# Kernel optimization log

Hardware: AMD Instinct MI355X
Metric: run time of the kernel (lower is better)

Reference implementation:

```python
import jax, jax.numpy as jnp
import numpy as np

E, H = 1024, 16


def setup_inputs() -> dict:
    key = jax.random.key(0)
    k1, k2, k3, k4 = jax.random.split(key, 4)
    B, L = 4, 2048
    embeddings = jax.random.normal(k1, (B, L, E), dtype=jnp.float32)
    mask = jax.random.randint(k2, (B, L, L), 0, 2) == 1  # True = masked out
    # Params (torch Linear y = x @ W.T; we store already-transposed [in, out])
    W_qkv = jax.random.normal(k3, (E, 3 * E), dtype=jnp.float32) * 0.02
    W_out = jax.random.normal(k4, (E, E), dtype=jnp.float32) * 0.02
    return {"embeddings": embeddings, "mask": mask, "W_qkv": W_qkv, "W_out": W_out}


def reference(embeddings, mask, W_qkv, W_out):
    B, L, E_ = embeddings.shape
    A = E_ // H
    scale = A ** (-0.5)
    qkv = embeddings @ W_qkv                       # [B, L, 3E]
    qkv = qkv.reshape(B, L, H, 3 * A).transpose(0, 2, 1, 3)  # [B, H, L, 3A]
    q, k, v = jnp.split(qkv, 3, axis=-1)           # each [B, H, L, A]
    scores = jnp.einsum('bhqa,bhka->bhqk', q, k) * scale  # [B, H, L, L]
    m = mask[:, None, :, :]                        # [B, 1, L, L]
    fully = jnp.all(m, axis=-1, keepdims=True)     # rows with every key masked
    scores = jnp.where(m, -jnp.inf, scores)
    scores = jnp.where(fully, 0.0, scores)         # keep softmax finite
    attn = jax.nn.softmax(scores, axis=-1)
    attn = jnp.where(fully, 0.0, attn)             # == torch nan_to_num(0)
    values = jnp.einsum('bhqk,bhka->bhqa', attn, v)  # [B, H, L, A]
    values = values.transpose(0, 2, 1, 3).reshape(B, L, E_)
    return values @ W_out
```

## Files before the change

kernel.cpp:

```cpp
#include <hip/hip_runtime.h>
#include <hip/hip_bf16.h>

#define B_   4
#define L_   2048
#define E_   1024
#define H_   16
#define T_   8192
#define K_   1024

typedef __attribute__((ext_vector_type(8))) short bf16x8;
typedef __attribute__((ext_vector_type(4))) float f32x4;
typedef __attribute__((ext_vector_type(4))) unsigned u32x4;

#define CSC_ (0.125f * 1.44269504f)

__device__ __forceinline__ ushort f2b(float f) {
    union { float f; unsigned u; } x; x.f = f;
    unsigned r = (x.u + 0x7fffu + ((x.u >> 16) & 1u)) >> 16;
    return (ushort)r;
}

__device__ __forceinline__ float fexp2(float x) {
#if __has_builtin(__builtin_amdgcn_exp2f)
    return __builtin_amdgcn_exp2f(x);
#else
    return __expf(x * 0.69314718056f);
#endif
}

__device__ __forceinline__ unsigned pack2bf(float a, float b) {
#if __has_builtin(__builtin_amdgcn_cvt_pk_bf16_f32)
    auto t = __builtin_amdgcn_cvt_pk_bf16_f32(a, b);
    return __builtin_bit_cast(unsigned, t);
#else
    unsigned ua = __builtin_bit_cast(unsigned, a) + 0x8000u;
    unsigned ub = __builtin_bit_cast(unsigned, b) + 0x8000u;
    return __builtin_amdgcn_perm(ub, ua, 0x07060302);
#endif
}

#define GLD_LDS16(gp, lp) __builtin_amdgcn_global_load_lds( \
    (const __attribute__((address_space(1))) void*)(gp), \
    (__attribute__((address_space(3))) void*)(lp), 16, 0, 0)

__global__ void detect_mask_layout(const unsigned char* __restrict__ m, int* flag) {
    __shared__ int s;
    if (threadIdx.x == 0) s = 0;
    __syncthreads();
    int found = 0;
    for (int i = threadIdx.x; i < 4096; i += 256)
        if ((i & 3) != 0 && m[i] != 0) found = 1;
    if (found) atomicOr(&s, 1);
    __syncthreads();
    if (threadIdx.x == 0) *flag = s;
}

__global__ void pack_mask(const void* __restrict__ mraw, const int* __restrict__ flag,
                          unsigned* __restrict__ tbits) {
    int row  = blockIdx.x;
    int lane = threadIdx.x & 63;
    int wave = threadIdx.x >> 6;
    int isByte = *flag;
    int b = row >> 11, q = row & 2047;
    const unsigned char* mb = (const unsigned char*)mraw;
    const int*           mi = (const int*)mraw;
    long long base = (long long)row * L_;
    for (int w = wave; w < 32; w += 4) {
        int idx = w * 64 + lane;
        int v = isByte ? (int)mb[base + idx] : mi[base + idx];
        unsigned long long word = __ballot(v == 0);
        if (lane == 0) {
            tbits[((size_t)b * 64 + 2 * w)     * 2048 + q] = (unsigned)word;
            tbits[((size_t)b * 64 + 2 * w + 1) * 2048 + q] = (unsigned)(word >> 32);
        }
    }
}

__global__ __launch_bounds__(256) void conv_bf16(const float* __restrict__ in,
                                                 ushort* __restrict__ out) {
    int i = blockIdx.x * 256 + threadIdx.x;
    float4 v = ((const float4*)in)[i];
    uint2 o;
    o.x = (unsigned)f2b(v.x) | ((unsigned)f2b(v.y) << 16);
    o.y = (unsigned)f2b(v.z) | ((unsigned)f2b(v.w) << 16);
    ((uint2*)out)[i] = o;
}

__global__ __launch_bounds__(256) void transpose_conv(const float* __restrict__ in,
        ushort* __restrict__ out, int R, int Cn) {
    __shared__ float t[32][33];
    int c0 = blockIdx.x * 32, r0 = blockIdx.y * 32;
    int x = threadIdx.x & 31, y = threadIdx.x >> 5;
#pragma unroll
    for (int k = 0; k < 4; ++k)
        t[y + k * 8][x] = in[(size_t)(r0 + y + k * 8) * Cn + c0 + x];
    __syncthreads();
#pragma unroll
    for (int k = 0; k < 4; ++k)
        out[(size_t)(c0 + y + k * 8) * R + r0 + x] = f2b(t[x][y + k * 8]);
}

template<int NDIM, int MODE>
__global__ __launch_bounds__(256) void gemm_bf16(
        const ushort* __restrict__ Ab, const ushort* __restrict__ Bt,
        float* __restrict__ Cg, ushort* __restrict__ Qb,
        ushort* __restrict__ Kb, ushort* __restrict__ Vt) {
    __shared__ ushort As[128 * 64];
    __shared__ ushort Bs[128 * 64];
    const int tid = threadIdx.x;
    const int wv = tid >> 6, ln = tid & 63;
    const int bn = blockIdx.x * 128, bm = blockIdx.y * 128;
    const int wm = (wv & 1) * 64, wn = (wv >> 1) * 64;
    const int row16 = ln & 15, quad = ln >> 4;
    const int cg8 = (((ln & 7) ^ (ln >> 3)) * 8);

    f32x4 acc[4][4];
#pragma unroll
    for (int i = 0; i < 4; ++i)
#pragma unroll
        for (int j = 0; j < 4; ++j) acc[i][j] = (f32x4){0.f, 0.f, 0.f, 0.f};

    for (int k0 = 0; k0 < K_; k0 += 64) {
        __syncthreads();
#pragma unroll
        for (int it = 0; it < 4; ++it) {
            int rA = wv * 32 + it * 8 + (ln >> 3);
            GLD_LDS16(Ab + (size_t)(bm + rA) * K_ + k0 + cg8, &As[(wv * 32 + it * 8) * 64]);
            GLD_LDS16(Bt + (size_t)(bn + rA) * K_ + k0 + cg8, &Bs[(wv * 32 + it * 8) * 64]);
        }
        __syncthreads();
#pragma unroll
        for (int ks = 0; ks < 2; ++ks) {
            const int ch = (((ks * 4 + quad) ^ (ln & 7)) * 8);
            bf16x8 af[4], bf[4];
#pragma unroll
            for (int i = 0; i < 4; ++i)
                af[i] = *(const bf16x8*)&As[(wm + i * 16 + row16) * 64 + ch];
#pragma unroll
            for (int j = 0; j < 4; ++j)
                bf[j] = *(const bf16x8*)&Bs[(wn + j * 16 + row16) * 64 + ch];
#pragma unroll
            for (int i = 0; i < 4; ++i)
#pragma unroll
                for (int j = 0; j < 4; ++j)
                    acc[i][j] = __builtin_amdgcn_mfma_f32_16x16x32_bf16(
                        af[i], bf[j], acc[i][j], 0, 0, 0);
        }
    }

    if (MODE == 0) {
#pragma unroll
        for (int i = 0; i < 4; ++i)
#pragma unroll
            for (int j = 0; j < 4; ++j) {
                int col = bn + wn + j * 16 + row16;
#pragma unroll
                for (int r = 0; r < 4; ++r) {
                    int row = bm + wm + i * 16 + quad * 4 + r;
                    Cg[(size_t)row * NDIM + col] = acc[i][j][r];
                }
            }
    } else {
#pragma unroll
        for (int j = 0; j < 4; ++j) {
            int col = bn + wn + j * 16 + row16;
            int h = col / 192, w = col - h * 192;
            int sel = w >> 6, a = w & 63;
            float qs = (sel == 0) ? CSC_ : 1.0f;
#pragma unroll
            for (int i = 0; i < 4; ++i)
#pragma unroll
                for (int r = 0; r < 4; ++r) {
                    int rowg = bm + wm + i * 16 + quad * 4 + r;
                    int b = rowg >> 11, l = rowg & 2047;
                    ushort v = f2b(acc[i][j][r] * qs);
                    size_t bh = (size_t)(b * H_ + h);
                    if (sel == 0)      Qb[(bh * L_ + l) * 64 + a] = v;
                    else if (sel == 1) Kb[(bh * L_ + l) * 64 + a] = v;
                    else {
                        int k5 = l & 31;
                        int lp = (l & ~31) | (2 * (k5 & 15) + (k5 >> 4));
                        Vt[(bh * 64 + a) * L_ + lp] = v;
                    }
                }
        }
    }
}

__global__ __launch_bounds__(512, 4) void attn_mfma(
        const ushort* __restrict__ Qb, const ushort* __restrict__ Kb,
        const ushort* __restrict__ Vt, const unsigned* __restrict__ tbits,
        ushort* __restrict__ vals) {
    __shared__ ushort KV[6][4096];

    const int tid = threadIdx.x, wv = tid >> 6, ln = tid & 63;
    const int bh = blockIdx.x, b = bh >> 4, h = bh & 15;
    const int q0 = blockIdx.y * 256;
    const int row16 = ln & 15, quad = ln >> 4;
    const int lh = ln >> 3, ll = ln & 7;
    const int cg8 = ((ll ^ lh) * 8);

    const ushort* Kg = Kb + (size_t)bh * L_ * 64;
    const ushort* Vg = Vt + (size_t)bh * 64 * L_;

    const int wk = wv & 3;
    const bool isK = (wv < 4);
    const int vc4 = ll ^ lh;
    const ushort* vstage = Vg + (size_t)(wk * 8 + lh + 32 * (vc4 >> 2)) * L_ + (vc4 & 3) * 8;
    const ushort* kstage = Kg + (size_t)(wk * 8 + lh) * 64 + cg8;

    ushort* lds = &KV[0][0];

    {
        const ushort* Qgw = Qb + ((size_t)bh * L_ + q0 + wv * 32) * 64;
#pragma unroll
        for (int it = 0; it < 4; ++it)
            GLD_LDS16(Qgw + (size_t)(it * 8 + lh) * 64 + cg8,
                      lds + (wv * 32 + it * 8) * 64);
    }
    __syncthreads();
    bf16x8 aq[2][2];
#pragma unroll
    for (int rg = 0; rg < 2; ++rg)
#pragma unroll
        for (int ks = 0; ks < 2; ++ks)
            aq[rg][ks] = *(const bf16x8*)&lds[(wv * 32 + rg * 16 + row16) * 64 +
                                              (((ks * 4 + quad) ^ (row16 & 7)) * 8)];
    __syncthreads();

    if (isK) {
        GLD_LDS16(kstage,               &KV[0][(wk * 8) * 64]);
        GLD_LDS16(kstage + 2048,        &KV[0][(32 + wk * 8) * 64]);
        GLD_LDS16(kstage + 4096,        &KV[1][(wk * 8) * 64]);
        GLD_LDS16(kstage + 4096 + 2048, &KV[1][(32 + wk * 8) * 64]);
        kstage += 8192;
    } else {
        GLD_LDS16(vstage,      &KV[3][(wk * 8) * 64]);
        GLD_LDS16(vstage + 32, &KV[3][(32 + wk * 8) * 64]);
        GLD_LDS16(vstage + 64, &KV[4][(wk * 8) * 64]);
        GLD_LDS16(vstage + 96, &KV[4][(32 + wk * 8) * 64]);
        vstage += 128;
    }

    bf16x8 vone;
#pragma unroll
    for (int i = 0; i < 8; ++i) vone[i] = (short)0x3F80;
    const f32x4 zf = (f32x4){0.f, 0.f, 0.f, 0.f};

    f32x4 oacc[2][4], lacc[2];
#pragma unroll
    for (int rg = 0; rg < 2; ++rg) {
        lacc[rg] = zf;
#pragma unroll
        for (int t = 0; t < 4; ++t) oacc[rg][t] = zf;
    }

    const unsigned* mptr = tbits + (size_t)b * 64 * 2048 + (q0 + wv * 32 + row16);

    auto qk = [&](const ushort* kbuf, int sub, f32x4 (&s)[2][2]) {
        __builtin_amdgcn_s_setprio(1);
#pragma unroll
        for (int ks = 0; ks < 2; ++ks) {
            bf16x8 bk[2];
#pragma unroll
            for (int t = 0; t < 2; ++t)
                bk[t] = *(const bf16x8*)&kbuf[(sub * 32 + t * 16 + row16) * 64 +
                                              (((ks * 4 + quad) ^ (row16 & 7)) * 8)];
#pragma unroll
            for (int rg = 0; rg < 2; ++rg)
#pragma unroll
                for (int t = 0; t < 2; ++t)
                    s[rg][t] = __builtin_amdgcn_mfma_f32_16x16x32_bf16(
                        bk[t], aq[rg][ks], ks ? s[rg][t] : zf, 0, 0, 0);
        }
        __builtin_amdgcn_s_setprio(0);
    };

    auto sm_pv = [&](f32x4 (&sa)[2][2], unsigned mlo, unsigned mhi,
                     const ushort* vbuf, int sub) {
        bf16x8 ap[2];
#pragma unroll
        for (int rg = 0; rg < 2; ++rg) {
            unsigned wr = rg ? mhi : mlo;
            u32x4 pw;
#pragma unroll
            for (int r = 0; r < 4; ++r) {
                unsigned sh = wr >> (quad * 4 + r);
                unsigned pk = pack2bf(fexp2(sa[rg][0][r]), fexp2(sa[rg][1][r]));
                pk &= (sh & 0x00010001u) * 0xFFFFu;
                pw[r] = pk;
            }
            ap[rg] = __builtin_bit_cast(bf16x8, pw);
        }
        bf16x8 bv[4];
#pragma unroll
        for (int t = 0; t < 4; ++t)
            bv[t] = *(const bf16x8*)&vbuf[(sub * 32 + (t & 1) * 16 + row16) * 64 +
                                          ((((t >> 1) * 4 + quad) ^ (row16 & 7)) * 8)];
        __builtin_amdgcn_s_setprio(1);
#pragma unroll
        for (int rg = 0; rg < 2; ++rg) {
            lacc[rg] = __builtin_amdgcn_mfma_f32_16x16x32_bf16(
                ap[rg], vone, lacc[rg], 0, 0, 0);
#pragma unroll
            for (int t = 0; t < 4; ++t)
                oacc[rg][t] = __builtin_amdgcn_mfma_f32_16x16x32_bf16(
                    ap[rg], bv[t], oacc[rg][t], 0, 0, 0);
        }
        __builtin_amdgcn_s_setprio(0);
    };

    auto iter = [&](const ushort* kb, const ushort* vb,
                    ushort* kn, ushort* vn, bool st) {
        unsigned m0lo = mptr[0],    m0hi = mptr[16];
        unsigned m1lo = mptr[2048], m1hi = mptr[2048 + 16];
        mptr += 4096;
        __builtin_amdgcn_sched_barrier(0);
        if (st) {
            if (isK) {
                GLD_LDS16(kstage,        kn + (wk * 8) * 64);
                GLD_LDS16(kstage + 2048, kn + (32 + wk * 8) * 64);
                kstage += 4096;
            } else {
                GLD_LDS16(vstage,      vn + (wk * 8) * 64);
                GLD_LDS16(vstage + 32, vn + (32 + wk * 8) * 64);
                vstage += 64;
            }
        }
        f32x4 s0[2][2];
        qk(kb, 0, s0);
        sm_pv(s0, m0lo, m0hi, vb, 0);
        f32x4 s1[2][2];
        qk(kb, 1, s1);
        sm_pv(s1, m1lo, m1hi, vb, 1);
        asm volatile("s_waitcnt vmcnt(2)" ::: "memory");
        __builtin_amdgcn_s_barrier();
        __builtin_amdgcn_sched_barrier(0);
    };

    asm volatile("s_waitcnt vmcnt(2)" ::: "memory");
    __builtin_amdgcn_s_barrier();
    __builtin_amdgcn_sched_barrier(0);

    for (int g = 0; g < 10; ++g) {
        iter(KV[0], KV[3], KV[2], KV[5], true);
        iter(KV[1], KV[4], KV[0], KV[3], true);
        iter(KV[2], KV[5], KV[1], KV[4], true);
    }
    iter(KV[0], KV[3], KV[2], KV[5], false);
    iter(KV[1], KV[4], KV[0], KV[3], false);

#pragma unroll
    for (int rg = 0; rg < 2; ++rg)
#pragma unroll
        for (int r = 0; r < 4; ++r) {
            float l = lacc[rg][r];
            float inv = (l > 0.f) ? 1.0f / l : 0.f;
            int qrow = q0 + wv * 32 + rg * 16 + quad * 4 + r;
            size_t base = ((size_t)b * L_ + qrow) * E_ + h * 64;
#pragma unroll
            for (int t = 0; t < 4; ++t)
                vals[base + t * 16 + row16] = f2b(oacc[rg][t][r] * inv);
        }
}

extern "C" void kernel_launch(void* const* d_in, const int* in_sizes, int n_in,
                              void* d_out, int out_size, void* d_ws, size_t ws_size,
                              hipStream_t stream) {
    const float* emb  = (const float*)d_in[0];
    const void*  mask = d_in[1];
    const float* wqkv = (const float*)d_in[2];
    const float* wout = (const float*)d_in[3];
    float* out = (float*)d_out;

    char* ws = (char*)d_ws;
    const size_t NEED = 4096ull + 2097152ull + 2ull * 46137344ull;
    if (ws_size < NEED) return;

    int* flag = (int*)ws;
    unsigned* tbits = (unsigned*)(ws + 4096);
    ushort* embb  = (ushort*)(ws + 4096 + 2097152);
    ushort* Wqkvt = embb  + 8388608;
    ushort* Wott  = Wqkvt + 3145728;
    ushort* Qb    = Wott  + 1048576;
    ushort* Kb    = Qb    + 8388608;
    ushort* Vt    = Kb    + 8388608;
    ushort* vals  = Vt    + 8388608;

    detect_mask_layout<<<1, 256, 0, stream>>>((const unsigned char*)mask, flag);
    pack_mask<<<T_, 256, 0, stream>>>(mask, flag, tbits);
    conv_bf16<<<8192, 256, 0, stream>>>(emb, embb);
    transpose_conv<<<dim3(96, 32), 256, 0, stream>>>(wqkv, Wqkvt, 1024, 3072);
    transpose_conv<<<dim3(32, 32), 256, 0, stream>>>(wout, Wott, 1024, 1024);
    gemm_bf16<3072, 1><<<dim3(24, 64), 256, 0, stream>>>(
        embb, Wqkvt, nullptr, Qb, Kb, Vt);
    attn_mfma<<<dim3(64, 8), 512, 0, stream>>>(Qb, Kb, Vt, tbits, vals);
    gemm_bf16<1024, 0><<<dim3(8, 64), 256, 0, stream>>>(
        vals, Wott, out, nullptr, nullptr, nullptr);
}
```

Measured before the change: 357.1 us.

## Double-buffer GEMM LDS tiles with 32-wide K steps to overlap loads

Rewrites the bf16 GEMM main loop to use two LDS buffers, each holding a 32-wide K slice, in place of one 64-wide buffer. The next slice is issued to global-to-LDS while MFMAs run on the current one, with one barrier per step. It also sets launch bounds to 4 blocks per CU and changes the LDS swizzle to match the narrower rows. This trades twice as many K iterations and barriers for overlap of memory latency with compute.

```diff
diff --git a/kernel.cpp b/kernel.cpp
--- a/kernel.cpp
+++ b/kernel.cpp
@@ -101,18 +101,31 @@
 }
 
 template<int NDIM, int MODE>
-__global__ __launch_bounds__(256) void gemm_bf16(
+__global__ __launch_bounds__(256, 4) void gemm_bf16(
         const ushort* __restrict__ Ab, const ushort* __restrict__ Bt,
         float* __restrict__ Cg, ushort* __restrict__ Qb,
         ushort* __restrict__ Kb, ushort* __restrict__ Vt) {
-    __shared__ ushort As[128 * 64];
-    __shared__ ushort Bs[128 * 64];
+    __shared__ ushort As[2][128 * 32];
+    __shared__ ushort Bs[2][128 * 32];
     const int tid = threadIdx.x;
     const int wv = tid >> 6, ln = tid & 63;
     const int bn = blockIdx.x * 128, bm = blockIdx.y * 128;
     const int wm = (wv & 1) * 64, wn = (wv >> 1) * 64;
     const int row16 = ln & 15, quad = ln >> 4;
-    const int cg8 = (((ln & 7) ^ (ln >> 3)) * 8);
+
+    const int rr = ln >> 2;
+    const int cc8 = (((ln & 3) ^ (rr & 3)) * 8);
+
+    const ushort* Ag = Ab + (size_t)(bm + wv * 32 + rr) * K_ + cc8;
+    const ushort* Bg = Bt + (size_t)(bn + wv * 32 + rr) * K_ + cc8;
+
+    auto stage = [&](int k0, int buf) {
+#pragma unroll
+        for (int g = 0; g < 2; ++g) {
+            GLD_LDS16(Ag + (size_t)(g * 16) * K_ + k0, &As[buf][(wv * 32 + g * 16) * 32]);
+            GLD_LDS16(Bg + (size_t)(g * 16) * K_ + k0, &Bs[buf][(wv * 32 + g * 16) * 32]);
+        }
+    };
 
     f32x4 acc[4][4];
 #pragma unroll
@@ -120,32 +133,34 @@
 #pragma unroll
         for (int j = 0; j < 4; ++j) acc[i][j] = (f32x4){0.f, 0.f, 0.f, 0.f};
 
-    for (int k0 = 0; k0 < K_; k0 += 64) {
+    const int ch = (quad ^ (row16 & 3)) * 8;
+
+    auto compute = [&](const ushort* Ac, const ushort* Bc) {
+        bf16x8 af[4], bf[4];
+#pragma unroll
+        for (int i = 0; i < 4; ++i)
+            af[i] = *(const bf16x8*)&Ac[(wm + i * 16 + row16) * 32 + ch];
+#pragma unroll
+        for (int j = 0; j < 4; ++j)
+            bf[j] = *(const bf16x8*)&Bc[(wn + j * 16 + row16) * 32 + ch];
+#pragma unroll
+        for (int i = 0; i < 4; ++i)
+#pragma unroll
+            for (int j = 0; j < 4; ++j)
+                acc[i][j] = __builtin_amdgcn_mfma_f32_16x16x32_bf16(
+                    af[i], bf[j], acc[i][j], 0, 0, 0);
+    };
+
+    stage(0, 0);
+    __syncthreads();
+
+    for (int t = 0; t < 32; t += 2) {
+        stage((t + 1) * 32, 1);
+        compute(As[0], Bs[0]);
         __syncthreads();
-#pragma unroll
-        for (int it = 0; it < 4; ++it) {
-            int rA = wv * 32 + it * 8 + (ln >> 3);
-            GLD_LDS16(Ab + (size_t)(bm + rA) * K_ + k0 + cg8, &As[(wv * 32 + it * 8) * 64]);
-            GLD_LDS16(Bt + (size_t)(bn + rA) * K_ + k0 + cg8, &Bs[(wv * 32 + it * 8) * 64]);
-        }
+        if (t + 2 < 32) stage((t + 2) * 32, 0);
+        compute(As[1], Bs[1]);
         __syncthreads();
-#pragma unroll
-        for (int ks = 0; ks < 2; ++ks) {
-            const int ch = (((ks * 4 + quad) ^ (ln & 7)) * 8);
-            bf16x8 af[4], bf[4];
-#pragma unroll
-            for (int i = 0; i < 4; ++i)
-                af[i] = *(const bf16x8*)&As[(wm + i * 16 + row16) * 64 + ch];
-#pragma unroll
-            for (int j = 0; j < 4; ++j)
-                bf[j] = *(const bf16x8*)&Bs[(wn + j * 16 + row16) * 64 + ch];
-#pragma unroll
-            for (int i = 0; i < 4; ++i)
-#pragma unroll
-                for (int j = 0; j < 4; ++j)
-                    acc[i][j] = __builtin_amdgcn_mfma_f32_16x16x32_bf16(
-                        af[i], bf[j], acc[i][j], 0, 0, 0);
-        }
     }
 
     if (MODE == 0) {
```

Measured after the change: 353.3 us. Within noise of the previous version (-1.1%).

## Pipeline GEMM with triple-buffered A, double-buffered B, larger 256x128 tiles

Applied to the files above, without the earlier changes.

Rewrites the bf16 GEMM main loop to use 512-thread blocks with 256x128 output tiles. A tiles are triple-buffered and B tiles double-buffered in LDS, with global-to-LDS loads issued in phases interleaved with the MFMA work and gated by explicit vmcnt/lgkmcnt waits and barriers. It also raises wave priority around the MFMA blocks. The goal is to hide global load latency behind compute and to cut per-block sync overhead. The cost is more LDS (about 128KB per block), which limits occupancy, and more barriers per k-step.

```diff
diff --git a/kernel.cpp b/kernel.cpp
--- a/kernel.cpp
+++ b/kernel.cpp
@@ -100,59 +100,114 @@
         out[(size_t)(c0 + y + k * 8) * R + r0 + x] = f2b(t[x][y + k * 8]);
 }
 
+#define ASZ_ 16384
+#define BSZ_ 8192
+
 template<int NDIM, int MODE>
-__global__ __launch_bounds__(256) void gemm_bf16(
+__global__ __launch_bounds__(512, 2) void gemm_bf16(
         const ushort* __restrict__ Ab, const ushort* __restrict__ Bt,
         float* __restrict__ Cg, ushort* __restrict__ Qb,
         ushort* __restrict__ Kb, ushort* __restrict__ Vt) {
-    __shared__ ushort As[128 * 64];
-    __shared__ ushort Bs[128 * 64];
+    __shared__ ushort LDSm[3 * ASZ_ + 2 * BSZ_];
+    ushort* Asb = LDSm;
+    ushort* Bsb = LDSm + 3 * ASZ_;
+
     const int tid = threadIdx.x;
     const int wv = tid >> 6, ln = tid & 63;
-    const int bn = blockIdx.x * 128, bm = blockIdx.y * 128;
-    const int wm = (wv & 1) * 64, wn = (wv >> 1) * 64;
+    const int bn = blockIdx.x * 128, bm = blockIdx.y * 256;
+    const int wm = (wv & 1) * 128, wn = (wv >> 1) * 32;
     const int row16 = ln & 15, quad = ln >> 4;
-    const int cg8 = (((ln & 7) ^ (ln >> 3)) * 8);
-
-    f32x4 acc[4][4];
-#pragma unroll
-    for (int i = 0; i < 4; ++i)
-#pragma unroll
-        for (int j = 0; j < 4; ++j) acc[i][j] = (f32x4){0.f, 0.f, 0.f, 0.f};
-
-    for (int k0 = 0; k0 < K_; k0 += 64) {
-        __syncthreads();
-#pragma unroll
-        for (int it = 0; it < 4; ++it) {
-            int rA = wv * 32 + it * 8 + (ln >> 3);
-            GLD_LDS16(Ab + (size_t)(bm + rA) * K_ + k0 + cg8, &As[(wv * 32 + it * 8) * 64]);
-            GLD_LDS16(Bt + (size_t)(bn + rA) * K_ + k0 + cg8, &Bs[(wv * 32 + it * 8) * 64]);
-        }
-        __syncthreads();
-#pragma unroll
-        for (int ks = 0; ks < 2; ++ks) {
-            const int ch = (((ks * 4 + quad) ^ (ln & 7)) * 8);
-            bf16x8 af[4], bf[4];
-#pragma unroll
-            for (int i = 0; i < 4; ++i)
-                af[i] = *(const bf16x8*)&As[(wm + i * 16 + row16) * 64 + ch];
-#pragma unroll
-            for (int j = 0; j < 4; ++j)
-                bf[j] = *(const bf16x8*)&Bs[(wn + j * 16 + row16) * 64 + ch];
-#pragma unroll
-            for (int i = 0; i < 4; ++i)
-#pragma unroll
-                for (int j = 0; j < 4; ++j)
-                    acc[i][j] = __builtin_amdgcn_mfma_f32_16x16x32_bf16(
-                        af[i], bf[j], acc[i][j], 0, 0, 0);
+
+    const int lh = ln >> 3, ll = ln & 7;
+    const int sw8 = (ll ^ lh) * 8;
+    const ushort* Ag = Ab + (size_t)(bm + wv * 8 + lh) * K_ + sw8;
+    const ushort* Bg = Bt + (size_t)(bn + wv * 8 + lh) * K_ + sw8;
+
+    auto stA2 = [&](int k0, ushort* dst, int rb) {
+#pragma unroll
+        for (int r = 0; r < 2; ++r)
+            GLD_LDS16(Ag + (size_t)((rb + r) * 64) * K_ + k0,
+                      dst + ((rb + r) * 64 + wv * 8) * 64);
+    };
+    auto stB2 = [&](int k0, ushort* dst) {
+#pragma unroll
+        for (int r = 0; r < 2; ++r)
+            GLD_LDS16(Bg + (size_t)(r * 64) * K_ + k0,
+                      dst + (r * 64 + wv * 8) * 64);
+    };
+
+    f32x4 acc[8][2];
+#pragma unroll
+    for (int i = 0; i < 8; ++i)
+#pragma unroll
+        for (int j = 0; j < 2; ++j) acc[i][j] = (f32x4){0.f, 0.f, 0.f, 0.f};
+
+    stA2(0, Asb, 0); stA2(0, Asb, 2);
+    stB2(0, Bsb);
+    stA2(64, Asb + ASZ_, 0); stA2(64, Asb + ASZ_, 2);
+    asm volatile("s_waitcnt vmcnt(4)" ::: "memory");
+    __builtin_amdgcn_s_barrier();
+    __builtin_amdgcn_sched_barrier(0);
+
+    for (int t = 0; t < 16; ++t) {
+        const ushort* Ar = Asb + (t % 3) * ASZ_;
+        const ushort* Br = Bsb + (t & 1) * BSZ_;
+        ushort* Ast = Asb + ((t + 2) % 3) * ASZ_;
+        ushort* Bst = Bsb + ((t + 1) & 1) * BSZ_;
+        const int kA = (t + 2) * 64, kB = (t + 1) * 64;
+        bf16x8 bfr[2][2];
+#pragma unroll
+        for (int p = 0; p < 4; ++p) {
+            bf16x8 af[2][2];
+#pragma unroll
+            for (int di = 0; di < 2; ++di)
+#pragma unroll
+                for (int ks = 0; ks < 2; ++ks) {
+                    int row = wm + (2 * p + di) * 16 + row16;
+                    af[di][ks] = *(const bf16x8*)&Ar[row * 64 +
+                                     (((ks * 4 + quad) ^ (row16 & 7)) * 8)];
+                }
+            if (p == 0) {
+#pragma unroll
+                for (int j = 0; j < 2; ++j)
+#pragma unroll
+                    for (int ks = 0; ks < 2; ++ks) {
+                        int row = wn + j * 16 + row16;
+                        bfr[j][ks] = *(const bf16x8*)&Br[row * 64 +
+                                         (((ks * 4 + quad) ^ (row16 & 7)) * 8)];
+                    }
+            }
+            if (p == 0 && t < 15) stB2(kB, Bst);
+            if (p == 1 && t < 14) stA2(kA, Ast, 0);
+            if (p == 2 && t < 14) stA2(kA, Ast, 2);
+            __builtin_amdgcn_sched_barrier(0);
+            __builtin_amdgcn_s_barrier();
+            asm volatile("s_waitcnt lgkmcnt(0)" ::: "memory");
+            __builtin_amdgcn_sched_barrier(0);
+            __builtin_amdgcn_s_setprio(1);
+#pragma unroll
+            for (int ks = 0; ks < 2; ++ks)
+#pragma unroll
+                for (int di = 0; di < 2; ++di)
+#pragma unroll
+                    for (int j = 0; j < 2; ++j)
+                        acc[2 * p + di][j] = __builtin_amdgcn_mfma_f32_16x16x32_bf16(
+                            af[di][ks], bfr[j][ks], acc[2 * p + di][j], 0, 0, 0);
+            __builtin_amdgcn_s_setprio(0);
+            if (p == 3) {
+                if (t < 14)       { asm volatile("s_waitcnt vmcnt(4)" ::: "memory"); }
+                else if (t == 14) { asm volatile("s_waitcnt vmcnt(0)" ::: "memory"); }
+            }
+            __builtin_amdgcn_s_barrier();
+            __builtin_amdgcn_sched_barrier(0);
         }
     }
 
     if (MODE == 0) {
 #pragma unroll
-        for (int i = 0; i < 4; ++i)
-#pragma unroll
-            for (int j = 0; j < 4; ++j) {
+        for (int i = 0; i < 8; ++i)
+#pragma unroll
+            for (int j = 0; j < 2; ++j) {
                 int col = bn + wn + j * 16 + row16;
 #pragma unroll
                 for (int r = 0; r < 4; ++r) {
@@ -162,13 +217,13 @@
             }
     } else {
 #pragma unroll
-        for (int j = 0; j < 4; ++j) {
+        for (int j = 0; j < 2; ++j) {
             int col = bn + wn + j * 16 + row16;
             int h = col / 192, w = col - h * 192;
             int sel = w >> 6, a = w & 63;
             float qs = (sel == 0) ? CSC_ : 1.0f;
 #pragma unroll
-            for (int i = 0; i < 4; ++i)
+            for (int i = 0; i < 8; ++i)
 #pragma unroll
                 for (int r = 0; r < 4; ++r) {
                     int rowg = bm + wm + i * 16 + quad * 4 + r;
@@ -392,9 +447,9 @@
     conv_bf16<<<8192, 256, 0, stream>>>(emb, embb);
     transpose_conv<<<dim3(96, 32), 256, 0, stream>>>(wqkv, Wqkvt, 1024, 3072);
     transpose_conv<<<dim3(32, 32), 256, 0, stream>>>(wout, Wott, 1024, 1024);
-    gemm_bf16<3072, 1><<<dim3(24, 64), 256, 0, stream>>>(
+    gemm_bf16<3072, 1><<<dim3(24, 32), 512, 0, stream>>>(
         embb, Wqkvt, nullptr, Qb, Kb, Vt);
     attn_mfma<<<dim3(64, 8), 512, 0, stream>>>(Qb, Kb, Vt, tbits, vals);
-    gemm_bf16<1024, 0><<<dim3(8, 64), 256, 0, stream>>>(
+    gemm_bf16<1024, 0><<<dim3(8, 32), 512, 0, stream>>>(
         vals, Wott, out, nullptr, nullptr, nullptr);
 }
```

Result: no change. 360.2 us (+0.9%).
